# Kernel optimization log

Hardware: AMD Instinct MI355X
Metric: run time of the kernel (lower is better)

The kernel has to match this reference:

```python
import jax, jax.numpy as jnp
import numpy as np

D, H, L, P = 256, 8, 3, 4
DH = D // H
SHAPES = np.array([[72, 96], [36, 48], [18, 24]], dtype=np.int64)
STARTS = np.array([0, 72 * 96, 72 * 96 + 36 * 48], dtype=np.int64)
NV = int((SHAPES[:, 0] * SHAPES[:, 1]).sum())  # 9072


def layer_norm(x, s, b):
    m = x.mean(-1, keepdims=True)
    v = ((x - m) ** 2).mean(-1, keepdims=True)
    return (x - m) / jnp.sqrt(v + 1e-5) * s + b


def bilinear(v, loc, Hl, Wl):
    # v: [B,H,Hl*Wl,dh]; loc: [B,Lq,H,P,2] normalized in [0,1]
    B, nH, _, dh = v.shape
    Lq, nP = loc.shape[1], loc.shape[3]
    x = loc[..., 0] * Wl - 0.5  # grid_sample align_corners=False
    y = loc[..., 1] * Hl - 0.5
    x0 = jnp.floor(x); y0 = jnp.floor(y)
    wx = x - x0; wy = y - y0

    def gather(xi, yi, w):
        valid = (xi >= 0) & (xi < Wl) & (yi >= 0) & (yi < Hl)  # padding_mode='zeros'
        xi_c = jnp.clip(xi, 0, Wl - 1).astype(jnp.int32)
        yi_c = jnp.clip(yi, 0, Hl - 1).astype(jnp.int32)
        idx = jnp.transpose(yi_c * Wl + xi_c, (0, 2, 1, 3)).reshape(B, nH, Lq * nP)
        g = jnp.take_along_axis(v, idx[..., None], axis=2).reshape(B, nH, Lq, nP, dh)
        m = (jnp.transpose(valid, (0, 2, 1, 3)).astype(v.dtype) * jnp.transpose(w, (0, 2, 1, 3)))[..., None]
        return g * m

    return (gather(x0, y0, (1 - wx) * (1 - wy)) + gather(x0 + 1, y0, wx * (1 - wy))
            + gather(x0, y0 + 1, (1 - wx) * wy) + gather(x0 + 1, y0 + 1, wx * wy))


def ms_deform_attn(query, value_in, spatial_shapes, level_start_index, key_padding_mask,
                   ref, off_w, off_b, aw_w, aw_b, vproj_w, vproj_b, oproj_w, oproj_b):
    B, Lq, _ = query.shape
    off = (query @ off_w + off_b).reshape(B, Lq, H, L, P, 2)
    aw = jax.nn.softmax((query @ aw_w + aw_b).reshape(B, Lq, H, L * P), axis=-1).reshape(B, Lq, H, L, P)
    # normalizer is [W_l, H_l] per level
    normalizer = jnp.asarray(np.stack([SHAPES[:, 1], SHAPES[:, 0]], axis=-1), dtype=query.dtype)  # [L,2]
    loc = ref[:, :, None, :, None, :] + off / normalizer[None, None, None, :, None, :]  # [B,Lq,H,L,P,2]
    value = value_in @ vproj_w + vproj_b
    value = jnp.where(key_padding_mask[:, :, None], 0.0, value)
    value = value.reshape(B, -1, H, DH).transpose(0, 2, 1, 3)  # [B,H,Nv,dh]
    acc = 0.0
    for l in range(L):
        Hl, Wl = int(spatial_shapes[l][0]), int(spatial_shapes[l][1])
        st = int(level_start_index[l])
        v_l = value[:, :, st:st + Hl * Wl]
        sampled = bilinear(v_l, loc[:, :, :, l], Hl, Wl)  # [B,H,Lq,P,dh]
        acc = acc + (sampled * jnp.transpose(aw[:, :, :, l], (0, 2, 1, 3))[..., None]).sum(axis=3)
    ctx = acc.transpose(0, 2, 1, 3).reshape(B, Lq, D)
    return ctx @ oproj_w + oproj_b


def mha(q_in, kv_in, key_padding_mask, qw, qb, kw, kb, vw, vb, ow, ob):
    B, Lq, _ = q_in.shape
    Lk = kv_in.shape[1]
    q = (q_in @ qw + qb).reshape(B, Lq, H, DH)
    k = (kv_in @ kw + kb).reshape(B, Lk, H, DH)
    v = (kv_in @ vw + vb).reshape(B, Lk, H, DH)
    scores = jnp.einsum('bqhd,bkhd->bhqk', q, k) / jnp.sqrt(jnp.asarray(DH, q.dtype))
    scores = jnp.where(key_padding_mask[:, None, None, :], -1e9, scores)
    a = jax.nn.softmax(scores, axis=-1)
    ctx = jnp.einsum('bhqk,bkhd->bqhd', a, v).reshape(B, Lq, D)
    return ctx @ ow + ob


def _forward(vis_tokens, text_tokens, vis_value,
             ref_w, ref_b, off_w, off_b, aw_w, aw_b, vproj_w, vproj_b, oproj_w, oproj_b,
             lvi_out_w, lvi_out_b, lvi_n1_s, lvi_n1_b, lvi_f1_w, lvi_f1_b, lvi_f2_w, lvi_f2_b, lvi_n2_s, lvi_n2_b,
             mha_qw, mha_qb, mha_kw, mha_kb, mha_vw, mha_vb, mha_ow, mha_ob,
             vli_out_w, vli_out_b, vli_n1_s, vli_n1_b, vli_f1_w, vli_f1_b, vli_f2_w, vli_f2_b, vli_n2_s, vli_n2_b,
             spatial_shapes, level_start_index, text_padding_mask, vis_key_padding_mask):
    B, Lt, _ = text_tokens.shape
    # --- DeformLVI: text queries multi-scale visual features ---
    ref = jax.nn.sigmoid(text_tokens @ ref_w + ref_b).reshape(B, Lt, L, 2)
    ctx = ms_deform_attn(text_tokens, vis_value, spatial_shapes, level_start_index, vis_key_padding_mask,
                         ref, off_w, off_b, aw_w, aw_b, vproj_w, vproj_b, oproj_w, oproj_b)
    t = layer_norm(text_tokens + ctx @ lvi_out_w + lvi_out_b, lvi_n1_s, lvi_n1_b)
    ffn = jax.nn.relu(t @ lvi_f1_w + lvi_f1_b) @ lvi_f2_w + lvi_f2_b
    text_out = layer_norm(t + ffn, lvi_n2_s, lvi_n2_b)
    # --- VLI: visual tokens query enriched text ---
    ctx_v = mha(vis_tokens, text_out, text_padding_mask, mha_qw, mha_qb, mha_kw, mha_kb, mha_vw, mha_vb, mha_ow, mha_ob)
    v = layer_norm(vis_tokens + ctx_v @ vli_out_w + vli_out_b, vli_n1_s, vli_n1_b)
    ffn_v = jax.nn.relu(v @ vli_f1_w + vli_f1_b) @ vli_f2_w + vli_f2_b
    vis_out = layer_norm(v + ffn_v, vli_n2_s, vli_n2_b)
    return vis_out, text_out


def setup_inputs() -> dict:
    key = jax.random.key(0)
    ks = iter(jax.random.split(key, 64))
    B, Lt = 8, 32
    w = lambda i, o: jax.random.normal(next(ks), (i, o), jnp.float32) * 0.02
    z = lambda o: jnp.zeros((o,), jnp.float32)
    inp = {
        'vis_tokens': jax.random.normal(next(ks), (B, NV, D), jnp.float32),
        'text_tokens': jax.random.normal(next(ks), (B, Lt, D), jnp.float32),
        'vis_value': jax.random.normal(next(ks), (B, NV, D), jnp.float32),
        'ref_w': w(D, L * 2), 'ref_b': z(L * 2),
        'off_w': w(D, H * L * P * 2), 'off_b': z(H * L * P * 2),
        'aw_w': w(D, H * L * P), 'aw_b': z(H * L * P),
        'vproj_w': w(D, D), 'vproj_b': z(D),
        'oproj_w': w(D, D), 'oproj_b': z(D),
        'lvi_out_w': w(D, D), 'lvi_out_b': z(D),
        'lvi_n1_s': jnp.ones((D,), jnp.float32), 'lvi_n1_b': z(D),
        'lvi_f1_w': w(D, 4 * D), 'lvi_f1_b': z(4 * D),
        'lvi_f2_w': w(4 * D, D), 'lvi_f2_b': z(D),
        'lvi_n2_s': jnp.ones((D,), jnp.float32), 'lvi_n2_b': z(D),
        'mha_qw': w(D, D), 'mha_qb': z(D),
        'mha_kw': w(D, D), 'mha_kb': z(D),
        'mha_vw': w(D, D), 'mha_vb': z(D),
        'mha_ow': w(D, D), 'mha_ob': z(D),
        'vli_out_w': w(D, D), 'vli_out_b': z(D),
        'vli_n1_s': jnp.ones((D,), jnp.float32), 'vli_n1_b': z(D),
        'vli_f1_w': w(D, 4 * D), 'vli_f1_b': z(4 * D),
        'vli_f2_w': w(4 * D, D), 'vli_f2_b': z(D),
        'vli_n2_s': jnp.ones((D,), jnp.float32), 'vli_n2_b': z(D),
        'spatial_shapes': SHAPES,
        'level_start_index': STARTS,
        'text_padding_mask': jnp.zeros((B, Lt), bool),
        'vis_key_padding_mask': jnp.zeros((B, NV), bool),
    }
    return inp


def reference(vis_tokens, text_tokens, vis_value,
              ref_w, ref_b, off_w, off_b, aw_w, aw_b, vproj_w, vproj_b, oproj_w, oproj_b,
              lvi_out_w, lvi_out_b, lvi_n1_s, lvi_n1_b, lvi_f1_w, lvi_f1_b, lvi_f2_w, lvi_f2_b, lvi_n2_s, lvi_n2_b,
              mha_qw, mha_qb, mha_kw, mha_kb, mha_vw, mha_vb, mha_ow, mha_ob,
              vli_out_w, vli_out_b, vli_n1_s, vli_n1_b, vli_f1_w, vli_f1_b, vli_f2_w, vli_f2_b, vli_n2_s, vli_n2_b,
              spatial_shapes, level_start_index, text_padding_mask, vis_key_padding_mask):
    return _forward(vis_tokens, text_tokens, vis_value,
                    ref_w, ref_b, off_w, off_b, aw_w, aw_b, vproj_w, vproj_b, oproj_w, oproj_b,
                    lvi_out_w, lvi_out_b, lvi_n1_s, lvi_n1_b, lvi_f1_w, lvi_f1_b, lvi_f2_w, lvi_f2_b, lvi_n2_s, lvi_n2_b,
                    mha_qw, mha_qb, mha_kw, mha_kb, mha_vw, mha_vb, mha_ow, mha_ob,
                    vli_out_w, vli_out_b, vli_n1_s, vli_n1_b, vli_f1_w, vli_f1_b, vli_f2_w, vli_f2_b, vli_n2_s, vli_n2_b,
                    spatial_shapes, level_start_index, text_padding_mask, vis_key_padding_mask)
```

## Files before the change

### kernel.cpp

```cpp
#include <hip/hip_runtime.h>
#include <hip/hip_bf16.h>
#include <math.h>

typedef __hip_bfloat16 bf16;
typedef unsigned short ushort_t;
typedef unsigned int uint_t;
typedef short v8s __attribute__((ext_vector_type(8)));
typedef float v4f __attribute__((ext_vector_type(4)));

#define NVTOK 9072
#define BATCH 8
#define LT 32
#define DMODEL 256
#define NHEAD 8
#define DHEAD 32
#define MVIS (BATCH*NVTOK)
#define MTEXT (BATCH*LT)
#define VISSZ 18579456ull

__device__ __forceinline__ float bf2f(ushort_t u){ return __uint_as_float(((uint_t)u)<<16); }
__device__ __forceinline__ ushort_t f2bfbits(float f){
  __hip_bfloat16 h = __float2bfloat16(f);
  union { __hip_bfloat16 h; ushort_t u; } c; c.h = h; return c.u;
}
__device__ __forceinline__ float ldin(const void* p, size_t i, int mode){
  return mode ? ((const float*)p)[i] : bf2f(((const ushort_t*)p)[i]);
}
__device__ __forceinline__ void stout(void* p, size_t i, int mode, float v){
  if (mode) ((float*)p)[i] = v; else ((ushort_t*)p)[i] = f2bfbits(v);
}

__global__ void k_detect(const uint_t* __restrict__ buf, int n_avail, int* __restrict__ flag){
  __shared__ int zc, bc;
  if (threadIdx.x==0){ zc=0; bc=0; }
  __syncthreads();
  int stride = n_avail/2048; if (stride < 1) stride = 1;
  int nz=0, nb=0;
  for (int i=threadIdx.x; i<2048; i+=256){
    long long idx = (long long)i*stride;
    if (idx >= n_avail) break;
    uint_t d = buf[idx];
    uint_t lo = d & 0xFFFFu;
    int e = (int)((lo >> 7) & 0xFF);
    if (lo == 0) nz++;
    else if (e >= 90 && e <= 160) nb++;
  }
  atomicAdd(&zc, nz); atomicAdd(&bc, nb);
  __syncthreads();
  if (threadIdx.x==0){
    int mode;
    if (zc > 1024) mode = 1;
    else if (bc > 1228) mode = 0;
    else mode = 1;
    *flag = mode;
  }
}

__global__ __launch_bounds__(256) void k_transpose(
    const void* W, ushort_t* __restrict__ Wt, int K, int N,
    const int* __restrict__ mf)
{
  const int mode = *mf;
  __shared__ float tile[32][33];
  const int k0 = blockIdx.x*32, n0 = blockIdx.y*32;
  const int c = threadIdx.x & 31, r8 = threadIdx.x >> 5;
  #pragma unroll
  for (int i=0;i<4;i++){
    const int kk = r8 + i*8;
    tile[kk][c] = ldin(W, (size_t)(k0+kk)*N + n0 + c, mode);
  }
  __syncthreads();
  #pragma unroll
  for (int i=0;i<4;i++){
    const int nn = r8 + i*8;
    Wt[(size_t)(n0+nn)*K + k0 + c] = f2bfbits(tile[c][nn]);
  }
}

__global__ __launch_bounds__(256) void k_text_prep(
    const void* text,
    const void* ref_w, const void* ref_b,
    const void* off_w, const void* off_b,
    const void* aw_w,  const void* aw_b,
    float* __restrict__ loc_out, float* __restrict__ aw_out,
    const int* __restrict__ mf)
{
  const int mode = *mf;
  const int r = blockIdx.x;
  const int t = threadIdx.x;
  __shared__ float x[256];
  __shared__ float refv[6];
  __shared__ float offv[192];
  __shared__ float logit[96];
  x[t] = ldin(text, (size_t)r*256 + t, mode);
  __syncthreads();
  if (t < 192) {
    float s = 0.f;
    for (int k=0;k<256;k++) s += x[k]*ldin(off_w, (size_t)k*192+t, mode);
    offv[t] = s + ldin(off_b, t, mode);
  } else if (t < 198) {
    int j = t-192;
    float s = 0.f;
    for (int k=0;k<256;k++) s += x[k]*ldin(ref_w, (size_t)k*6+j, mode);
    s += ldin(ref_b, j, mode);
    refv[j] = 1.f/(1.f+expf(-s));
  }
  if (t < 96) {
    float s = 0.f;
    for (int k=0;k<256;k++) s += x[k]*ldin(aw_w, (size_t)k*96+t, mode);
    logit[t] = s + ldin(aw_b, t, mode);
  }
  __syncthreads();
  if (t < 8) {
    float mx = -1e30f;
    for (int j=0;j<12;j++) mx = fmaxf(mx, logit[t*12+j]);
    float e[12]; float den = 0.f;
    for (int j=0;j<12;j++){ e[j] = expf(logit[t*12+j]-mx); den += e[j]; }
    float inv = 1.f/den;
    for (int j=0;j<12;j++) aw_out[(size_t)r*96 + t*12 + j] = e[j]*inv;
  }
  if (t < 192) {
    int rem = t % 24;
    int l = rem >> 3;
    int c = t & 1;
    const float normW[3] = {96.f,48.f,24.f};
    const float normH[3] = {72.f,36.f,18.f};
    float nrm = (c==0) ? normW[l] : normH[l];
    loc_out[(size_t)r*192 + t] = refv[l*2+c] + offv[t]/nrm;
  }
}

__global__ __launch_bounds__(64) void k_deform(
    const void* vis_value, const char* __restrict__ vmask,
    const void* vproj_w, const void* vproj_b,
    const float* __restrict__ loc, const float* __restrict__ aw,
    float* __restrict__ ctx_out, const int* __restrict__ mf)
{
  const int mode = *mf;
  const int blk = blockIdx.x;
  const int r = blk >> 3;
  const int h = blk & 7;
  const int b = r >> 5;
  const int t = threadIdx.x;
  const int Hs[3] = {72,36,18};
  const int Wsz[3] = {96,48,24};
  const int stl[3] = {0,6912,8640};
  float s0=0.f,s1=0.f,s2=0.f,s3=0.f, wsum=0.f;
  for (int l=0;l<3;l++){
    for (int p=0;p<4;p++){
      const int sIdx = blk*12 + l*4 + p;
      const float a  = aw[sIdx];
      const float X = loc[sIdx*2+0]*(float)Wsz[l] - 0.5f;
      const float Y = loc[sIdx*2+1]*(float)Hs[l] - 0.5f;
      const float x0f = floorf(X), y0f = floorf(Y);
      const int x0 = (int)x0f, y0 = (int)y0f;
      const float wx = X-x0f, wy = Y-y0f;
      const float cw[4] = {(1.f-wx)*(1.f-wy), wx*(1.f-wy), (1.f-wx)*wy, wx*wy};
      const int cx[4] = {x0,x0+1,x0,x0+1};
      const int cy[4] = {y0,y0,y0+1,y0+1};
      for (int c=0;c<4;c++){
        if (cx[c]>=0 && cx[c]<Wsz[l] && cy[c]>=0 && cy[c]<Hs[l]){
          const size_t pos = (size_t)b*NVTOK + stl[l] + cy[c]*Wsz[l] + cx[c];
          if (vmask[pos]) continue;
          const float w = a*cw[c];
          wsum += w;
          const size_t base = pos*256 + t*4;
          s0 += w*ldin(vis_value, base+0, mode);
          s1 += w*ldin(vis_value, base+1, mode);
          s2 += w*ldin(vis_value, base+2, mode);
          s3 += w*ldin(vis_value, base+3, mode);
        }
      }
    }
  }
  __shared__ float sh[256];
  sh[t*4+0]=s0; sh[t*4+1]=s1; sh[t*4+2]=s2; sh[t*4+3]=s3;
  __syncthreads();
  if (t < 32) {
    const int col = h*32 + t;
    float acc = wsum * ldin(vproj_b, col, mode);
    for (int k=0;k<256;k++) acc += sh[k]*ldin(vproj_w, (size_t)k*256+col, mode);
    ctx_out[(size_t)r*256 + col] = acc;
  }
}

__device__ __forceinline__ float block_sum(float v, float* red){
  float sm = v;
  #pragma unroll
  for (int o=32;o>0;o>>=1) sm += __shfl_down(sm,o);
  const int t = threadIdx.x;
  __syncthreads();
  if ((t&63)==0) red[t>>6] = sm;
  __syncthreads();
  return red[0]+red[1]+red[2]+red[3];
}

__global__ __launch_bounds__(256) void k_mgemm(
    const void* A, size_t a_off, int a_kind,
    const ushort_t* __restrict__ Wt, const void* bias, float* __restrict__ C,
    int N, int K, int relu, const int* __restrict__ mf)
{
  const int mode = *mf;
  const int split = (a_kind==1) || (mode==1);
  __shared__ ushort_t Ah[128*32];
  __shared__ ushort_t Al[128*32];
  __shared__ ushort_t Bt[128*32];
  const int tid = threadIdx.x;
  const int gm0 = blockIdx.x*128, gn0 = blockIdx.y*128;
  const int wv = tid>>6, lane = tid&63;
  const int mh = (wv&1)*64, nh = (wv>>1)*64;
  const int r16 = lane&15, q8 = (lane>>4)*8;
  const int srow = tid>>1, sseg = (tid&1)*16;
  v4f acc[4][4];
  #pragma unroll
  for (int i=0;i<4;i++)
    #pragma unroll
    for (int j=0;j<4;j++) acc[i][j] = (v4f){0.f,0.f,0.f,0.f};

  for (int k0=0; k0<K; k0+=32){
    if (k0) __syncthreads();
    {
      const ushort_t* src = Wt + (size_t)(gn0+srow)*K + k0 + sseg;
      ((uint4*)&Bt[srow*32+sseg])[0]   = ((const uint4*)src)[0];
      ((uint4*)&Bt[srow*32+sseg+8])[0] = ((const uint4*)src)[1];
    }
    if (!split){
      const ushort_t* src = (const ushort_t*)A + a_off + (size_t)(gm0+srow)*K + k0 + sseg;
      ((uint4*)&Ah[srow*32+sseg])[0]   = ((const uint4*)src)[0];
      ((uint4*)&Ah[srow*32+sseg+8])[0] = ((const uint4*)src)[1];
    } else {
      const float* src = (const float*)A + a_off + (size_t)(gm0+srow)*K + k0 + sseg;
      #pragma unroll
      for (int v=0;v<4;v++){
        float4 f = ((const float4*)src)[v];
        float xs[4] = {f.x, f.y, f.z, f.w};
        #pragma unroll
        for (int e=0;e<4;e++){
          const int idx = srow*32 + sseg + v*4 + e;
          const ushort_t h = f2bfbits(xs[e]);
          Ah[idx] = h;
          Al[idx] = f2bfbits(xs[e] - bf2f(h));
        }
      }
    }
    __syncthreads();
    v8s af[4], bfr[4], al[4];
    #pragma unroll
    for (int mt=0;mt<4;mt++){
      af[mt] = *(const v8s*)&Ah[(mh + mt*16 + r16)*32 + q8];
      if (split) al[mt] = *(const v8s*)&Al[(mh + mt*16 + r16)*32 + q8];
    }
    #pragma unroll
    for (int nt=0;nt<4;nt++)
      bfr[nt] = *(const v8s*)&Bt[(nh + nt*16 + r16)*32 + q8];
    #pragma unroll
    for (int mt=0;mt<4;mt++){
      #pragma unroll
      for (int nt=0;nt<4;nt++){
        acc[mt][nt] = __builtin_amdgcn_mfma_f32_16x16x32_bf16(af[mt], bfr[nt], acc[mt][nt], 0, 0, 0);
        if (split)
          acc[mt][nt] = __builtin_amdgcn_mfma_f32_16x16x32_bf16(al[mt], bfr[nt], acc[mt][nt], 0, 0, 0);
      }
    }
  }
  const int rq = (lane>>4)*4;
  float bv[4];
  #pragma unroll
  for (int nt=0;nt<4;nt++) bv[nt] = ldin(bias, gn0 + nh + nt*16 + r16, mode);
  #pragma unroll
  for (int mt=0;mt<4;mt++){
    #pragma unroll
    for (int r=0;r<4;r++){
      const size_t ro = (size_t)(gm0 + mh + mt*16 + rq + r)*N + gn0 + nh + r16;
      #pragma unroll
      for (int nt=0;nt<4;nt++){
        float v = acc[mt][nt][r] + bv[nt];
        if (relu) v = fmaxf(v, 0.f);
        C[ro + nt*16] = v;
      }
    }
  }
}

__global__ __launch_bounds__(256) void k_kvsplit(
    const float* __restrict__ kws, const float* __restrict__ vws,
    ushort_t* __restrict__ khi, ushort_t* __restrict__ klo,
    ushort_t* __restrict__ vthi, ushort_t* __restrict__ vtlo)
{
  const int row = blockIdx.x;
  const int b = row >> 5, key = row & 31;
  const int t = threadIdx.x;
  const float f = kws[(size_t)row*256 + t];
  const ushort_t fh = f2bfbits(f);
  khi[(size_t)row*256 + t] = fh;
  klo[(size_t)row*256 + t] = f2bfbits(f - bf2f(fh));
  const float g = vws[(size_t)row*256 + t];
  const ushort_t gh = f2bfbits(g);
  const size_t vt = ((size_t)b*256 + t)*32 + key;
  vthi[vt] = gh;
  vtlo[vt] = f2bfbits(g - bf2f(gh));
}

__global__ __launch_bounds__(256) void k_attn2(
    float* __restrict__ qc,
    const ushort_t* __restrict__ khi, const ushort_t* __restrict__ klo,
    const ushort_t* __restrict__ vthi, const ushort_t* __restrict__ vtlo,
    const char* __restrict__ tmask, int r0)
{
  __shared__ float P[4][16][36];
  const int tid = threadIdx.x;
  const int wv = tid>>6, lane = tid&63;
  const int lrow0 = blockIdx.x*64 + wv*16;
  const int b = (r0 + lrow0)/NVTOK;
  const int m16 = lane&15;
  const int kq = lane>>4;
  const int q8 = kq*8;
  const int key0 = m16, key1 = m16+16;
  const bool msk0 = tmask[b*LT + key0] != 0;
  const bool msk1 = tmask[b*LT + key1] != 0;
  const float scale = 0.17677669529663687f;

  for (int h=0; h<8; ++h){
    const float* qrow = qc + (size_t)(lrow0 + m16)*256 + h*32 + q8;
    float qv[8];
    *(float4*)&qv[0] = *(const float4*)&qrow[0];
    *(float4*)&qv[4] = *(const float4*)&qrow[4];
    v8s qh, ql;
    #pragma unroll
    for (int j=0;j<8;j++){
      const ushort_t hb = f2bfbits(qv[j]);
      qh[j] = (short)hb;
      ql[j] = (short)f2bfbits(qv[j] - bf2f(hb));
    }
    const size_t kb0 = ((size_t)(b*32+key0)*256) + h*32 + q8;
    const size_t kb1 = ((size_t)(b*32+key1)*256) + h*32 + q8;
    const v8s kh0 = *(const v8s*)&khi[kb0];
    const v8s kl0 = *(const v8s*)&klo[kb0];
    const v8s kh1 = *(const v8s*)&khi[kb1];
    const v8s kl1 = *(const v8s*)&klo[kb1];
    v4f s0 = (v4f){0.f,0.f,0.f,0.f}, s1 = (v4f){0.f,0.f,0.f,0.f};
    s0 = __builtin_amdgcn_mfma_f32_16x16x32_bf16(qh, kh0, s0, 0,0,0);
    s0 = __builtin_amdgcn_mfma_f32_16x16x32_bf16(qh, kl0, s0, 0,0,0);
    s0 = __builtin_amdgcn_mfma_f32_16x16x32_bf16(ql, kh0, s0, 0,0,0);
    s1 = __builtin_amdgcn_mfma_f32_16x16x32_bf16(qh, kh1, s1, 0,0,0);
    s1 = __builtin_amdgcn_mfma_f32_16x16x32_bf16(qh, kl1, s1, 0,0,0);
    s1 = __builtin_amdgcn_mfma_f32_16x16x32_bf16(ql, kh1, s1, 0,0,0);
    float e0[4], e1[4], inv[4];
    #pragma unroll
    for (int r=0;r<4;r++){
      const float a0 = msk0 ? -1e9f : s0[r]*scale;
      const float a1 = msk1 ? -1e9f : s1[r]*scale;
      float mx = fmaxf(a0,a1);
      #pragma unroll
      for (int o=1;o<16;o<<=1) mx = fmaxf(mx, __shfl_xor(mx,o));
      const float x0 = __expf(a0-mx), x1 = __expf(a1-mx);
      float dn = x0+x1;
      #pragma unroll
      for (int o=1;o<16;o<<=1) dn += __shfl_xor(dn,o);
      e0[r]=x0; e1[r]=x1; inv[r] = 1.f/dn;
    }
    #pragma unroll
    for (int r=0;r<4;r++){
      P[wv][kq*4+r][key0] = e0[r];
      P[wv][kq*4+r][key1] = e1[r];
    }
    __syncthreads();
    float pv[8];
    *(float4*)&pv[0] = *(const float4*)&P[wv][m16][q8];
    *(float4*)&pv[4] = *(const float4*)&P[wv][m16][q8+4];
    v8s ph, pl;
    #pragma unroll
    for (int j=0;j<8;j++){
      const ushort_t hb = f2bfbits(pv[j]);
      ph[j] = (short)hb;
      pl[j] = (short)f2bfbits(pv[j] - bf2f(hb));
    }
    const size_t vb0 = ((size_t)(b*256 + h*32 + m16)*32) + q8;
    const size_t vb1 = ((size_t)(b*256 + h*32 + 16 + m16)*32) + q8;
    const v8s vh0 = *(const v8s*)&vthi[vb0];
    const v8s vl0 = *(const v8s*)&vtlo[vb0];
    const v8s vh1 = *(const v8s*)&vthi[vb1];
    const v8s vl1 = *(const v8s*)&vtlo[vb1];
    v4f o0 = (v4f){0.f,0.f,0.f,0.f}, o1 = (v4f){0.f,0.f,0.f,0.f};
    o0 = __builtin_amdgcn_mfma_f32_16x16x32_bf16(ph, vh0, o0, 0,0,0);
    o0 = __builtin_amdgcn_mfma_f32_16x16x32_bf16(ph, vl0, o0, 0,0,0);
    o0 = __builtin_amdgcn_mfma_f32_16x16x32_bf16(pl, vh0, o0, 0,0,0);
    o1 = __builtin_amdgcn_mfma_f32_16x16x32_bf16(ph, vh1, o1, 0,0,0);
    o1 = __builtin_amdgcn_mfma_f32_16x16x32_bf16(ph, vl1, o1, 0,0,0);
    o1 = __builtin_amdgcn_mfma_f32_16x16x32_bf16(pl, vh1, o1, 0,0,0);
    __syncthreads();
    #pragma unroll
    for (int r=0;r<4;r++){
      float* orow = qc + (size_t)(lrow0 + kq*4 + r)*256 + h*32;
      orow[m16]      = o0[r]*inv[r];
      orow[16 + m16] = o1[r]*inv[r];
    }
  }
}

__global__ __launch_bounds__(256) void k_add_ln(
    const float* __restrict__ X, const void* R, size_t r_off, int r_f32,
    void* OUT, size_t o_off, int o_f32,
    void* OUT2, size_t o2_off,
    const void* g, const void* be, const int* __restrict__ mf)
{
  const int mode = *mf;
  const int row = blockIdx.x; const int t = threadIdx.x;
  const size_t idx = (size_t)row*256 + t;
  __shared__ float red[4];
  const float rv = r_f32 ? ((const float*)R)[r_off+idx] : ldin(R, r_off+idx, mode);
  const float v = X[idx] + rv;
  const float m = block_sum(v, red) * (1.f/256.f);
  __syncthreads();
  const float d = v - m;
  const float var = block_sum(d*d, red) * (1.f/256.f);
  const float o = d*rsqrtf(var+1e-5f)*ldin(g,t,mode) + ldin(be,t,mode);
  if (o_f32) ((float*)OUT)[o_off+idx] = o;
  else       stout(OUT, o_off+idx, mode, o);
  if (OUT2)  stout(OUT2, o2_off+idx, mode, o);
}

extern "C" void kernel_launch(void* const* d_in, const int* in_sizes, int n_in,
                              void* d_out, int out_size, void* d_ws, size_t ws_size,
                              hipStream_t stream)
{
  (void)n_in; (void)out_size;
  const void* vis_tokens = d_in[0];
  const void* text_tokens= d_in[1];
  const void* vis_value  = d_in[2];
  const void* ref_w = d_in[3];  const void* ref_b = d_in[4];
  const void* off_w = d_in[5];  const void* off_b = d_in[6];
  const void* aw_w  = d_in[7];  const void* aw_b  = d_in[8];
  const void* vproj_w = d_in[9];  const void* vproj_b = d_in[10];
  const void* oproj_w = d_in[11]; const void* oproj_b = d_in[12];
  const void* lvi_out_w = d_in[13]; const void* lvi_out_b = d_in[14];
  const void* lvi_n1_s = d_in[15];  const void* lvi_n1_b = d_in[16];
  const void* lvi_f1_w = d_in[17];  const void* lvi_f1_b = d_in[18];
  const void* lvi_f2_w = d_in[19];  const void* lvi_f2_b = d_in[20];
  const void* lvi_n2_s = d_in[21];  const void* lvi_n2_b = d_in[22];
  const void* mha_qw = d_in[23]; const void* mha_qb = d_in[24];
  const void* mha_kw = d_in[25]; const void* mha_kb = d_in[26];
  const void* mha_vw = d_in[27]; const void* mha_vb = d_in[28];
  const void* mha_ow = d_in[29]; const void* mha_ob = d_in[30];
  const void* vli_out_w = d_in[31]; const void* vli_out_b = d_in[32];
  const void* vli_n1_s = d_in[33];  const void* vli_n1_b = d_in[34];
  const void* vli_f1_w = d_in[35];  const void* vli_f1_b = d_in[36];
  const void* vli_f2_w = d_in[37];  const void* vli_f2_b = d_in[38];
  const void* vli_n2_s = d_in[39];  const void* vli_n2_b = d_in[40];
  const char* tmask = (const char*)d_in[43];
  const char* vmask = (const char*)d_in[44];

  char* ws = (char*)d_ws;
  int*   flag    = (int*)  (ws + 0);
  float* loc_ws  = (float*)(ws + 256);
  float* aw_ws   = (float*)(ws + 196864);
  float* ctxt_ws = (float*)(ws + 295168);
  float* t_ws    = (float*)(ws + 557312);
  float* tout_ws = (float*)(ws + 819456);
  float* k_ws    = (float*)(ws + 1081600);
  float* v_ws    = (float*)(ws + 1343744);
  ushort_t* wtq  = (ushort_t*)(ws + 1605888ull);
  ushort_t* wto  = (ushort_t*)(ws + 1736960ull);
  ushort_t* wtf1 = (ushort_t*)(ws + 1868032ull);
  ushort_t* wtf2 = (ushort_t*)(ws + 2392320ull);
  ushort_t* wtk   = (ushort_t*)(ws + 2916608ull);
  ushort_t* wtv   = (ushort_t*)(ws + 3047680ull);
  ushort_t* wtop  = (ushort_t*)(ws + 3178752ull);
  ushort_t* wtlo  = (ushort_t*)(ws + 3309824ull);
  ushort_t* wtlf1 = (ushort_t*)(ws + 3440896ull);
  ushort_t* wtlf2 = (ushort_t*)(ws + 3965184ull);
  float* hbuf_t   = (float*)(ws + 4489472ull);
  float* ybuf     = (float*)(ws + 5538048ull);
  float* fbuf     = (float*)(ws + 5800192ull);
  ushort_t* khi   = (ushort_t*)(ws + 6062336ull);
  ushort_t* klo   = (ushort_t*)(ws + 6193408ull);
  ushort_t* vthi  = (ushort_t*)(ws + 6324480ull);
  ushort_t* vtlo  = (ushort_t*)(ws + 6455552ull);
  const size_t fe = 6586624ull;

  long long R_ll = 128;
  if (ws_size > fe) R_ll = (long long)((ws_size - fe) / 7168ull);
  if (R_ll > (long long)MVIS) R_ll = MVIS;
  R_ll &= ~127LL;
  if (R_ll < 128) R_ll = 128;
  const int R = (int)R_ll;
  float* qctx = (float*)(ws + fe);
  float* ubuf = (float*)(ws + fe + (size_t)R*1024ull);
  float* v1b  = (float*)(ws + fe + (size_t)R*2048ull);
  float* hbuf = (float*)(ws + fe + (size_t)R*3072ull);

  int ndw = in_sizes[1]/2; if (ndw < 1) ndw = 1;
  k_detect<<<1,256,0,stream>>>((const uint_t*)text_tokens, ndw, flag);

  k_transpose<<<dim3(8,8),  256,0,stream>>>(mha_qw,    wtq,   256, 256,  flag);
  k_transpose<<<dim3(8,8),  256,0,stream>>>(mha_ow,    wto,   256, 256,  flag);
  k_transpose<<<dim3(8,32), 256,0,stream>>>(vli_f1_w,  wtf1,  256, 1024, flag);
  k_transpose<<<dim3(32,8), 256,0,stream>>>(vli_f2_w,  wtf2,  1024, 256, flag);
  k_transpose<<<dim3(8,8),  256,0,stream>>>(mha_kw,    wtk,   256, 256,  flag);
  k_transpose<<<dim3(8,8),  256,0,stream>>>(mha_vw,    wtv,   256, 256,  flag);
  k_transpose<<<dim3(8,8),  256,0,stream>>>(oproj_w,   wtop,  256, 256,  flag);
  k_transpose<<<dim3(8,8),  256,0,stream>>>(lvi_out_w, wtlo,  256, 256,  flag);
  k_transpose<<<dim3(8,32), 256,0,stream>>>(lvi_f1_w,  wtlf1, 256, 1024, flag);
  k_transpose<<<dim3(32,8), 256,0,stream>>>(lvi_f2_w,  wtlf2, 1024, 256, flag);

  k_text_prep<<<MTEXT,256,0,stream>>>(text_tokens, ref_w, ref_b, off_w, off_b,
                                      aw_w, aw_b, loc_ws, aw_ws, flag);
  k_deform<<<MTEXT*NHEAD,64,0,stream>>>(vis_value, vmask, vproj_w, vproj_b,
                                        loc_ws, aw_ws, ctxt_ws, flag);

  {
    dim3 g22(2,2);
    k_mgemm<<<g22,256,0,stream>>>(ctxt_ws, 0, 1, wtop, oproj_b, ybuf, 256, 256, 0, flag);
    k_mgemm<<<g22,256,0,stream>>>(ybuf,    0, 1, wtlo, lvi_out_b, fbuf, 256, 256, 0, flag);
    k_add_ln<<<MTEXT,256,0,stream>>>(fbuf, text_tokens, 0, 0,
                                     t_ws, 0, 1, nullptr, 0, lvi_n1_s, lvi_n1_b, flag);
  }
  {
    dim3 g28(2,8), g22(2,2);
    k_mgemm<<<g28,256,0,stream>>>(t_ws,   0, 1, wtlf1, lvi_f1_b, hbuf_t, 1024, 256, 1, flag);
    k_mgemm<<<g22,256,0,stream>>>(hbuf_t, 0, 1, wtlf2, lvi_f2_b, fbuf,   256, 1024, 0, flag);
    k_add_ln<<<MTEXT,256,0,stream>>>(fbuf, t_ws, 0, 1,
                                     tout_ws, 0, 1, d_out, VISSZ, lvi_n2_s, lvi_n2_b, flag);
  }
  {
    dim3 g22(2,2);
    k_mgemm<<<g22,256,0,stream>>>(tout_ws, 0, 1, wtk, mha_kb, k_ws, 256, 256, 0, flag);
    k_mgemm<<<g22,256,0,stream>>>(tout_ws, 0, 1, wtv, mha_vb, v_ws, 256, 256, 0, flag);
    k_kvsplit<<<256,256,0,stream>>>(k_ws, v_ws, khi, klo, vthi, vtlo);
  }

  for (int r0 = 0; r0 < MVIS; r0 += R){
    const int nr = (MVIS - r0 < R) ? (MVIS - r0) : R;
    dim3 g2(nr/128, 2);
    k_mgemm<<<g2,256,0,stream>>>(vis_tokens, (size_t)r0*256, 0,
                                 wtq, mha_qb, qctx, 256, 256, 0, flag);
    k_attn2<<<nr/64,256,0,stream>>>(qctx, khi, klo, vthi, vtlo, tmask, r0);
    k_mgemm<<<g2,256,0,stream>>>(qctx, 0, 1, wto, mha_ob, ubuf, 256, 256, 0, flag);
    k_add_ln<<<nr,256,0,stream>>>(ubuf, vis_tokens, (size_t)r0*256, 0,
                                  v1b, 0, 1, nullptr, 0, vli_n1_s, vli_n1_b, flag);
    dim3 g8(nr/128, 8);
    k_mgemm<<<g8,256,0,stream>>>(v1b, 0, 1, wtf1, vli_f1_b, hbuf, 1024, 256, 1, flag);
    k_mgemm<<<g2,256,0,stream>>>(hbuf, 0, 1, wtf2, vli_f2_b, ubuf, 256, 1024, 0, flag);
    k_add_ln<<<nr,256,0,stream>>>(ubuf, v1b, 0, 1,
                                  d_out, (size_t)r0*256, 0, nullptr, 0, vli_n2_s, vli_n2_b, flag);
  }
}
```

Before: 1.062 ms.

## Store intermediate activations as bf16 hi/lo pairs to skip in-GEMM fp32 splitting

```diff
diff --git a/kernel.cpp b/kernel.cpp
--- a/kernel.cpp
+++ b/kernel.cpp
@@ -282,6 +282,115 @@
   }
 }
 
+__global__ __launch_bounds__(256) void k_mgemm2(
+    const void* A, size_t a_off, int a_kind,
+    const ushort_t* __restrict__ Alo_p,
+    const ushort_t* __restrict__ Wt, const void* bias,
+    float* __restrict__ Cf, ushort_t* __restrict__ Chi, ushort_t* __restrict__ Clo,
+    int N, int K, int relu, const int* __restrict__ mf)
+{
+  const int mode = *mf;
+  const int split = (a_kind==2) ? (Alo_p != nullptr) : (mode==1);
+  const int rawf32 = (a_kind==0) && (mode==1);
+  __shared__ ushort_t Ah[128*32];
+  __shared__ ushort_t Al[128*32];
+  __shared__ ushort_t Bt[128*32];
+  const int tid = threadIdx.x;
+  const int nbx = gridDim.x, nby = gridDim.y;
+  const int total = nbx*nby;
+  const int f = blockIdx.y*nbx + blockIdx.x;
+  const int qq = total>>3, rr = total&7;
+  const int xcd = f&7, pos = f>>3;
+  const int wg = (xcd<rr ? xcd*(qq+1) : rr*(qq+1) + (xcd-rr)*qq) + pos;
+  const int gm0 = (wg / nby)*128, gn0 = (wg % nby)*128;
+
+  const int wv = tid>>6, lane = tid&63;
+  const int mh = (wv&1)*64, nh = (wv>>1)*64;
+  const int r16 = lane&15, q8 = (lane>>4)*8;
+  const int srow = tid>>1, sseg = (tid&1)*16;
+  const ushort_t* Ahi_p = (const ushort_t*)A + a_off;
+  v4f acc[4][4];
+  #pragma unroll
+  for (int i=0;i<4;i++)
+    #pragma unroll
+    for (int j=0;j<4;j++) acc[i][j] = (v4f){0.f,0.f,0.f,0.f};
+
+  for (int k0=0; k0<K; k0+=32){
+    if (k0) __syncthreads();
+    {
+      const ushort_t* src = Wt + (size_t)(gn0+srow)*K + k0 + sseg;
+      ((uint4*)&Bt[srow*32+sseg])[0]   = ((const uint4*)src)[0];
+      ((uint4*)&Bt[srow*32+sseg+8])[0] = ((const uint4*)src)[1];
+    }
+    if (!rawf32){
+      const ushort_t* src = Ahi_p + (size_t)(gm0+srow)*K + k0 + sseg;
+      ((uint4*)&Ah[srow*32+sseg])[0]   = ((const uint4*)src)[0];
+      ((uint4*)&Ah[srow*32+sseg+8])[0] = ((const uint4*)src)[1];
+      if (split){
+        const ushort_t* srl = Alo_p + (size_t)(gm0+srow)*K + k0 + sseg;
+        ((uint4*)&Al[srow*32+sseg])[0]   = ((const uint4*)srl)[0];
+        ((uint4*)&Al[srow*32+sseg+8])[0] = ((const uint4*)srl)[1];
+      }
+    } else {
+      const float* src = (const float*)A + a_off + (size_t)(gm0+srow)*K + k0 + sseg;
+      #pragma unroll
+      for (int v=0;v<4;v++){
+        float4 fq = ((const float4*)src)[v];
+        float xs[4] = {fq.x, fq.y, fq.z, fq.w};
+        #pragma unroll
+        for (int e=0;e<4;e++){
+          const int idx = srow*32 + sseg + v*4 + e;
+          const ushort_t h = f2bfbits(xs[e]);
+          Ah[idx] = h;
+          Al[idx] = f2bfbits(xs[e] - bf2f(h));
+        }
+      }
+    }
+    __syncthreads();
+    v8s af[4], bfr[4], al[4];
+    #pragma unroll
+    for (int mt=0;mt<4;mt++){
+      af[mt] = *(const v8s*)&Ah[(mh + mt*16 + r16)*32 + q8];
+      if (split) al[mt] = *(const v8s*)&Al[(mh + mt*16 + r16)*32 + q8];
+    }
+    #pragma unroll
+    for (int nt=0;nt<4;nt++)
+      bfr[nt] = *(const v8s*)&Bt[(nh + nt*16 + r16)*32 + q8];
+    #pragma unroll
+    for (int mt=0;mt<4;mt++){
+      #pragma unroll
+      for (int nt=0;nt<4;nt++){
+        acc[mt][nt] = __builtin_amdgcn_mfma_f32_16x16x32_bf16(af[mt], bfr[nt], acc[mt][nt], 0, 0, 0);
+        if (split)
+          acc[mt][nt] = __builtin_amdgcn_mfma_f32_16x16x32_bf16(al[mt], bfr[nt], acc[mt][nt], 0, 0, 0);
+      }
+    }
+  }
+  const int rq = (lane>>4)*4;
+  float bv[4];
+  #pragma unroll
+  for (int nt=0;nt<4;nt++) bv[nt] = ldin(bias, gn0 + nh + nt*16 + r16, mode);
+  const int outf = (Cf != nullptr);
+  #pragma unroll
+  for (int mt=0;mt<4;mt++){
+    #pragma unroll
+    for (int r=0;r<4;r++){
+      const size_t ro = (size_t)(gm0 + mh + mt*16 + rq + r)*N + gn0 + nh + r16;
+      #pragma unroll
+      for (int nt=0;nt<4;nt++){
+        float v = acc[mt][nt][r] + bv[nt];
+        if (relu) v = fmaxf(v, 0.f);
+        if (outf) Cf[ro + nt*16] = v;
+        else {
+          const ushort_t hb = f2bfbits(v);
+          Chi[ro + nt*16] = hb;
+          Clo[ro + nt*16] = f2bfbits(v - bf2f(hb));
+        }
+      }
+    }
+  }
+}
+
 __global__ __launch_bounds__(256) void k_kvsplit(
     const float* __restrict__ kws, const float* __restrict__ vws,
     ushort_t* __restrict__ khi, ushort_t* __restrict__ klo,
@@ -302,7 +411,8 @@
 }
 
 __global__ __launch_bounds__(256) void k_attn2(
-    float* __restrict__ qc,
+    const float* __restrict__ qc,
+    ushort_t* __restrict__ aoh, ushort_t* __restrict__ aol,
     const ushort_t* __restrict__ khi, const ushort_t* __restrict__ klo,
     const ushort_t* __restrict__ vthi, const ushort_t* __restrict__ vtlo,
     const char* __restrict__ tmask, int r0)
@@ -391,9 +501,13 @@
     __syncthreads();
     #pragma unroll
     for (int r=0;r<4;r++){
-      float* orow = qc + (size_t)(lrow0 + kq*4 + r)*256 + h*32;
-      orow[m16]      = o0[r]*inv[r];
-      orow[16 + m16] = o1[r]*inv[r];
+      const size_t ro = (size_t)(lrow0 + kq*4 + r)*256 + h*32;
+      const float w0 = o0[r]*inv[r], w1 = o1[r]*inv[r];
+      const ushort_t h0 = f2bfbits(w0), h1 = f2bfbits(w1);
+      aoh[ro + m16]      = h0;
+      aol[ro + m16]      = f2bfbits(w0 - bf2f(h0));
+      aoh[ro + 16 + m16] = h1;
+      aol[ro + 16 + m16] = f2bfbits(w1 - bf2f(h1));
     }
   }
 }
@@ -418,6 +532,47 @@
   if (o_f32) ((float*)OUT)[o_off+idx] = o;
   else       stout(OUT, o_off+idx, mode, o);
   if (OUT2)  stout(OUT2, o2_off+idx, mode, o);
+}
+
+__global__ __launch_bounds__(256) void k_add_ln_pair(
+    const float* __restrict__ X, const void* R, size_t r_off,
+    ushort_t* __restrict__ OH, ushort_t* __restrict__ OL,
+    const void* g, const void* be, const int* __restrict__ mf)
+{
+  const int mode = *mf;
+  const int row = blockIdx.x; const int t = threadIdx.x;
+  const size_t idx = (size_t)row*256 + t;
+  __shared__ float red[4];
+  const float rv = ldin(R, r_off+idx, mode);
+  const float v = X[idx] + rv;
+  const float m = block_sum(v, red) * (1.f/256.f);
+  __syncthreads();
+  const float d = v - m;
+  const float var = block_sum(d*d, red) * (1.f/256.f);
+  const float o = d*rsqrtf(var+1e-5f)*ldin(g,t,mode) + ldin(be,t,mode);
+  const ushort_t hb = f2bfbits(o);
+  OH[idx] = hb;
+  OL[idx] = f2bfbits(o - bf2f(hb));
+}
+
+__global__ __launch_bounds__(256) void k_add_ln_pres(
+    const float* __restrict__ X,
+    const ushort_t* __restrict__ RH, const ushort_t* __restrict__ RL,
+    void* OUT, size_t o_off,
+    const void* g, const void* be, const int* __restrict__ mf)
+{
+  const int mode = *mf;
+  const int row = blockIdx.x; const int t = threadIdx.x;
+  const size_t idx = (size_t)row*256 + t;
+  __shared__ float red[4];
+  const float rv = bf2f(RH[idx]) + bf2f(RL[idx]);
+  const float v = X[idx] + rv;
+  const float m = block_sum(v, red) * (1.f/256.f);
+  __syncthreads();
+  const float d = v - m;
+  const float var = block_sum(d*d, red) * (1.f/256.f);
+  const float o = d*rsqrtf(var+1e-5f)*ldin(g,t,mode) + ldin(be,t,mode);
+  stout(OUT, o_off+idx, mode, o);
 }
 
 extern "C" void kernel_launch(void* const* d_in, const int* in_sizes, int n_in,
@@ -479,15 +634,19 @@
   const size_t fe = 6586624ull;
 
   long long R_ll = 128;
-  if (ws_size > fe) R_ll = (long long)((ws_size - fe) / 7168ull);
+  if (ws_size > fe) R_ll = (long long)((ws_size - fe) / 8192ull);
   if (R_ll > (long long)MVIS) R_ll = MVIS;
   R_ll &= ~127LL;
   if (R_ll < 128) R_ll = 128;
   const int R = (int)R_ll;
-  float* qctx = (float*)(ws + fe);
-  float* ubuf = (float*)(ws + fe + (size_t)R*1024ull);
-  float* v1b  = (float*)(ws + fe + (size_t)R*2048ull);
-  float* hbuf = (float*)(ws + fe + (size_t)R*3072ull);
+  float*    qctx = (float*)   (ws + fe);
+  float*    ubuf = (float*)   (ws + fe + (size_t)R*1024ull);
+  ushort_t* aoH  = (ushort_t*)(ws + fe + (size_t)R*2048ull);
+  ushort_t* aoL  = aoH + (size_t)R*256;
+  ushort_t* v1H  = (ushort_t*)(ws + fe + (size_t)R*3072ull);
+  ushort_t* v1L  = v1H + (size_t)R*256;
+  ushort_t* hbH  = (ushort_t*)(ws + fe + (size_t)R*4096ull);
+  ushort_t* hbL  = hbH + (size_t)R*1024;
 
   int ndw = in_sizes[1]/2; if (ndw < 1) ndw = 1;
   k_detect<<<1,256,0,stream>>>((const uint_t*)text_tokens, ndw, flag);
@@ -532,16 +691,19 @@
   for (int r0 = 0; r0 < MVIS; r0 += R){
     const int nr = (MVIS - r0 < R) ? (MVIS - r0) : R;
     dim3 g2(nr/128, 2);
-    k_mgemm<<<g2,256,0,stream>>>(vis_tokens, (size_t)r0*256, 0,
-                                 wtq, mha_qb, qctx, 256, 256, 0, flag);
-    k_attn2<<<nr/64,256,0,stream>>>(qctx, khi, klo, vthi, vtlo, tmask, r0);
-    k_mgemm<<<g2,256,0,stream>>>(qctx, 0, 1, wto, mha_ob, ubuf, 256, 256, 0, flag);
-    k_add_ln<<<nr,256,0,stream>>>(ubuf, vis_tokens, (size_t)r0*256, 0,
-                                  v1b, 0, 1, nullptr, 0, vli_n1_s, vli_n1_b, flag);
+    k_mgemm2<<<g2,256,0,stream>>>(vis_tokens, (size_t)r0*256, 0, nullptr,
+                                  wtq, mha_qb, qctx, nullptr, nullptr, 256, 256, 0, flag);
+    k_attn2<<<nr/64,256,0,stream>>>(qctx, aoH, aoL, khi, klo, vthi, vtlo, tmask, r0);
+    k_mgemm2<<<g2,256,0,stream>>>(aoH, 0, 2, aoL,
+                                  wto, mha_ob, ubuf, nullptr, nullptr, 256, 256, 0, flag);
+    k_add_ln_pair<<<nr,256,0,stream>>>(ubuf, vis_tokens, (size_t)r0*256,
+                                       v1H, v1L, vli_n1_s, vli_n1_b, flag);
     dim3 g8(nr/128, 8);
-    k_mgemm<<<g8,256,0,stream>>>(v1b, 0, 1, wtf1, vli_f1_b, hbuf, 1024, 256, 1, flag);
-    k_mgemm<<<g2,256,0,stream>>>(hbuf, 0, 1, wtf2, vli_f2_b, ubuf, 256, 1024, 0, flag);
-    k_add_ln<<<nr,256,0,stream>>>(ubuf, v1b, 0, 1,
-                                  d_out, (size_t)r0*256, 0, nullptr, 0, vli_n2_s, vli_n2_b, flag);
-  }
-}
+    k_mgemm2<<<g8,256,0,stream>>>(v1H, 0, 2, v1L,
+                                  wtf1, vli_f1_b, nullptr, hbH, hbL, 1024, 256, 1, flag);
+    k_mgemm2<<<g2,256,0,stream>>>(hbH, 0, 2, hbL,
+                                  wtf2, vli_f2_b, ubuf, nullptr, nullptr, 256, 1024, 0, flag);
+    k_add_ln_pres<<<nr,256,0,stream>>>(ubuf, v1H, v1L,
+                                       d_out, (size_t)r0*256, vli_n2_s, vli_n2_b, flag);
+  }
+}
```

New measurement: 1.231 ms. 1.16x slower.
